# Optimization experiments

Measured on AMD Instinct MI355X. Metric: run time of the kernel, lower is better.

## Reference

```python
import jax, jax.numpy as jnp
import numpy as np

VOCAB, EMB, HID, NCLS, B, T = 50000, 32, 64, 3, 512, 512

def setup_inputs() -> dict:
    key = jax.random.key(0)
    ks = jax.random.split(key, 7)
    tokens = jax.random.randint(ks[0], (B, T), 0, VOCAB, dtype=jnp.int32)
    emb = jax.random.normal(ks[1], (VOCAB, EMB), dtype=jnp.float32) * 0.05
    # Keras LSTM weights: kernel [EMB, 4*HID], recurrent_kernel [HID, 4*HID], bias [4*HID]; gate order i,f,c,o
    Wk = jax.random.normal(ks[2], (EMB, 4 * HID), dtype=jnp.float32) * (1.0 / np.sqrt(EMB))
    Wr = jax.random.normal(ks[3], (HID, 4 * HID), dtype=jnp.float32) * (1.0 / np.sqrt(HID))
    b = jnp.zeros((4 * HID,), dtype=jnp.float32)
    Wd = jax.random.normal(ks[4], (HID, NCLS), dtype=jnp.float32) * (1.0 / np.sqrt(HID))
    bd = jnp.zeros((NCLS,), dtype=jnp.float32)
    return {"tokens": tokens, "emb": emb, "Wk": Wk, "Wr": Wr, "b": b, "Wd": Wd, "bd": bd}

def _lstm_last_hidden(x, Wk, Wr, b):
    # x: [B, T, EMB] -> last hidden state [B, HID]. Keras gate order: i, f, c(g), o.
    Bsz = x.shape[0]
    # Precompute input projections for all timesteps (one big GEMM): [T, B, 4H]
    xz = jnp.einsum('bte,eh->tbh', x, Wk) + b

    def step(carry, xzt):
        h, c = carry
        z = xzt + h @ Wr  # [B, 4H]
        i, f, g, o = jnp.split(z, 4, axis=-1)
        i = jax.nn.sigmoid(i)
        f = jax.nn.sigmoid(f)
        o = jax.nn.sigmoid(o)
        c = f * c + i * jnp.tanh(g)
        h = o * jnp.tanh(c)
        return (h, c), None

    h0 = jnp.zeros((Bsz, HID), dtype=x.dtype)
    c0 = jnp.zeros((Bsz, HID), dtype=x.dtype)
    (hT, _), _ = jax.lax.scan(step, (h0, c0), xz)
    return hT

def reference(tokens, emb, Wk, Wr, b, Wd, bd):
    x = emb[tokens]                      # [B, T, EMB] embedding lookup
    h = _lstm_last_hidden(x, Wk, Wr, b)  # [B, HID]
    # Dropout layers are identity at inference; Dense + softmax
    logits = h @ Wd + bd                 # [B, NCLS]
    return jax.nn.softmax(logits, axis=-1)
```

## Files before the change

kernel.cpp:

```cpp
#include <hip/hip_runtime.h>


#define VOCAB 50000
#define EMB 32
#define HID 64
#define NCLS 3
#define BATCH 512
#define TSEQ 512
#define FOURH 256
#define LOG2E 1.4426950408889634f
#define GSEQ 4
#define NBLK (BATCH / GSEQ)

typedef _Float16 half8 __attribute__((ext_vector_type(8)));
typedef float f32x4 __attribute__((ext_vector_type(4)));

#define MFMA16 __builtin_amdgcn_mfma_f32_16x16x32_f16
#define PKRTZ(a, b) __builtin_bit_cast(int, __builtin_amdgcn_cvt_pkrtz((a), (b)))

#define WAVE_BARRIER()                                        \
    {                                                         \
        asm volatile("s_waitcnt lgkmcnt(0)" ::: "memory");    \
        __builtin_amdgcn_s_barrier();                         \
    }

#define LSTM_STEP(CUR, TT, XW, XL)                                            \
    {                                                                         \
        const half8* ap = (const half8*)(hxc + (CUR) * 768 + abase);          \
        const half8 a0 = ap[0];                                               \
        const half8 a1 = ap[4];                                               \
        const half8 a2 = ap[8];                                               \
        if (li8) {                                                            \
            int2 st;                                                          \
            st.x = PKRTZ(XW.x, XW.y);                                         \
            st.y = PKRTZ(XW.z, XW.w);                                         \
            *(int2*)(hxc + ((CUR) ^ 1) * 768 + xwoff) = st;                   \
            const int tn2 = ((TT) + 2 < TSEQ) ? (TT) + 2 : TSEQ - 1;          \
            const int tk = toks[(w << 9) + tn2];                              \
            XL = *(const float4*)(emb + tk * EMB + (l << 2));                 \
        }                                                                     \
        f32x4 A0, A1, A2, A3, B0, B1, B2, B3, C0, C1, C2, C3;                 \
        A0 = MFMA16(a0, bfr[0][0], zz, 0, 0, 0);                              \
        A1 = MFMA16(a0, bfr[1][0], zz, 0, 0, 0);                              \
        A2 = MFMA16(a0, bfr[2][0], zz, 0, 0, 0);                              \
        A3 = MFMA16(a0, bfr[3][0], zz, 0, 0, 0);                              \
        B0 = MFMA16(a1, bfr[0][1], zz, 0, 0, 0);                              \
        B1 = MFMA16(a1, bfr[1][1], zz, 0, 0, 0);                              \
        B2 = MFMA16(a1, bfr[2][1], zz, 0, 0, 0);                              \
        B3 = MFMA16(a1, bfr[3][1], zz, 0, 0, 0);                              \
        C0 = MFMA16(a2, bfr[0][2], zz, 0, 0, 0);                              \
        C1 = MFMA16(a2, bfr[1][2], zz, 0, 0, 0);                              \
        C2 = MFMA16(a2, bfr[2][2], zz, 0, 0, 0);                              \
        C3 = MFMA16(a2, bfr[3][2], zz, 0, 0, 0);                              \
        const float zi = (A0[0] + B0[0]) + C0[0];                             \
        const float zf = (A1[0] + B1[0]) + C1[0];                             \
        const float zg = (A2[0] + B2[0]) + C2[0];                             \
        const float zo = (A3[0] + B3[0]) + C3[0];                             \
        const float si = __builtin_amdgcn_rcpf(                               \
            1.0f + __builtin_amdgcn_exp2f(fmaf(zi, -LOG2E, bci)));            \
        const float sf = __builtin_amdgcn_rcpf(                               \
            1.0f + __builtin_amdgcn_exp2f(fmaf(zf, -LOG2E, bcf)));            \
        const float sg = __builtin_amdgcn_rcpf(                               \
            1.0f + __builtin_amdgcn_exp2f(fmaf(zg, -2.0f * LOG2E, bcg)));     \
        const float so = __builtin_amdgcn_rcpf(                               \
            1.0f + __builtin_amdgcn_exp2f(fmaf(zo, -LOG2E, bco)));            \
        const float gt = fmaf(2.0f, sg, -1.0f);                               \
        cst = fmaf(sf, cst, si * gt);                                         \
        const float st2 = __builtin_amdgcn_rcpf(                              \
            1.0f + __builtin_amdgcn_exp2f(cst * (-2.0f * LOG2E)));            \
        const float th = fmaf(2.0f, st2, -1.0f);                              \
        const float hv = so * th;                                             \
        *(_Float16*)(hxc + ((CUR) ^ 1) * 768 + hwoff) = (_Float16)hv;         \
        WAVE_BARRIER()                                                        \
    }

__global__ __launch_bounds__(256)
void lstm_kernel(const int* __restrict__ tokens, const float* __restrict__ emb,
                 const float* __restrict__ Wk, const float* __restrict__ Wr,
                 const float* __restrict__ bias, const float* __restrict__ Wd,
                 const float* __restrict__ bd, float* __restrict__ out)
{
    __shared__ __align__(16) _Float16 hx[2][GSEQ][96];
    __shared__ int toks[GSEQ * TSEQ];

    const int tid = threadIdx.x;
    const int w   = tid >> 6;
    const int l   = tid & 63;
    const int li  = l & 15;
    const int q   = l >> 4;
    const bool li8 = (l < 8);
    const int s0  = blockIdx.x << 2;

    char* hxc = (char*)&hx[0][0][0];

    {
        const int4* src = (const int4*)(tokens + (s0 << 9));
        int4* dst = (int4*)toks;
        dst[tid] = src[tid];
        dst[tid + 256] = src[tid + 256];
    }

    if (tid < 64) {
        int2 z2; z2.x = 0; z2.y = 0;
        *(int2*)(hxc + (tid >> 4) * 192 + ((tid & 15) << 3)) = z2;
    }

    half8 bfr[4][3];
#pragma unroll
    for (int g = 0; g < 4; ++g) {
        const int col = (g << 6) + (w << 4) + li;
#pragma unroll
        for (int c2 = 0; c2 < 3; ++c2) {
#pragma unroll
            for (int i = 0; i < 8; ++i) {
                const int k = (c2 << 5) + (q << 3) + i;
                const float wv = (k < HID) ? Wr[k * FOURH + col]
                                           : Wk[(k - HID) * FOURH + col];
                bfr[g][c2][i] = (_Float16)wv;
            }
        }
    }

    const int u = (w << 4) + li;
    const float bci = -bias[u] * LOG2E;
    const float bcf = -bias[u + 64] * LOG2E;
    const float bcg = -bias[u + 128] * (2.0f * LOG2E);
    const float bco = -bias[u + 192] * LOG2E;

    const int abase = ((li >> 2) * 192) + (q << 4);
    const int hwoff = q * 192 + (u << 1);
    const int xwoff = w * 192 + 128 + (l << 3);

    __syncthreads();

    float4 xA = make_float4(0.f, 0.f, 0.f, 0.f);
    float4 xB = make_float4(0.f, 0.f, 0.f, 0.f);
    if (li8) {
        const int tk0 = toks[w << 9];
        const float4 x0 = *(const float4*)(emb + tk0 * EMB + (l << 2));
        int2 st;
        st.x = PKRTZ(x0.x, x0.y);
        st.y = PKRTZ(x0.z, x0.w);
        *(int2*)(hxc + xwoff) = st;
        const int tk1 = toks[(w << 9) + 1];
        xA = *(const float4*)(emb + tk1 * EMB + (l << 2));
    }
    __syncthreads();

    float cst = 0.0f;
    const f32x4 zz = {0.0f, 0.0f, 0.0f, 0.0f};

    for (int t = 0; t < TSEQ; t += 2) {
        LSTM_STEP(0, t, xA, xB)
        LSTM_STEP(1, t + 1, xB, xA)
    }

    if (tid < GSEQ) {
        const _Float16* hf = &hx[0][tid][0];
        float a0 = bd[0], a1 = bd[1], a2 = bd[2];
#pragma unroll 8
        for (int k = 0; k < HID; ++k) {
            const float hk = (float)hf[k];
            a0 = fmaf(hk, Wd[k * NCLS + 0], a0);
            a1 = fmaf(hk, Wd[k * NCLS + 1], a1);
            a2 = fmaf(hk, Wd[k * NCLS + 2], a2);
        }
        const float mm = fmaxf(a0, fmaxf(a1, a2));
        const float e0 = __expf(a0 - mm);
        const float e1 = __expf(a1 - mm);
        const float e2 = __expf(a2 - mm);
        const float den = e0 + e1 + e2;
        float* op = out + (s0 + tid) * NCLS;
        op[0] = e0 / den;
        op[1] = e1 / den;
        op[2] = e2 / den;
    }
}

extern "C" void kernel_launch(void* const* d_in, const int* in_sizes, int n_in,
                              void* d_out, int out_size, void* d_ws, size_t ws_size,
                              hipStream_t stream) {
    const int*   tokens = (const int*)  d_in[0];
    const float* emb    = (const float*)d_in[1];
    const float* Wk     = (const float*)d_in[2];
    const float* Wr     = (const float*)d_in[3];
    const float* b      = (const float*)d_in[4];
    const float* Wd     = (const float*)d_in[5];
    const float* bd     = (const float*)d_in[6];
    float* out = (float*)d_out;
    (void)d_ws; (void)ws_size; (void)in_sizes; (void)n_in; (void)out_size;

    lstm_kernel<<<dim3(NBLK), dim3(256), 0, stream>>>(
        tokens, emb, Wk, Wr, b, Wd, bd, out);
}
```

Before: 240.7 us.

## Process two interleaved sequence groups per block to expose ILP in recurrence

Each block now handles 8 sequences as two independent groups of 4. Every wave interleaves the MFMA and activation chains of both groups, which halves the grid to 64 blocks. The MFMAs now accumulate through the C operand instead of summing three separate results. The aim is to hide MFMA and transcendental latency in the serial timestep loop by overlapping two independent recurrences, at the cost of doubled per-step work per wave and a longer dependent MFMA chain.

```diff
diff --git a/kernel.cpp b/kernel.cpp
--- a/kernel.cpp
+++ b/kernel.cpp
@@ -9,8 +9,9 @@
 #define TSEQ 512
 #define FOURH 256
 #define LOG2E 1.4426950408889634f
-#define GSEQ 4
+#define GSEQ 8
 #define NBLK (BATCH / GSEQ)
+#define GSTRIDE 1536
 
 typedef _Float16 half8 __attribute__((ext_vector_type(8)));
 typedef float f32x4 __attribute__((ext_vector_type(4)));
@@ -24,38 +25,8 @@
         __builtin_amdgcn_s_barrier();                         \
     }
 
-#define LSTM_STEP(CUR, TT, XW, XL)                                            \
+#define ACT(zi, zf, zg, zo, cst, hv)                                          \
     {                                                                         \
-        const half8* ap = (const half8*)(hxc + (CUR) * 768 + abase);          \
-        const half8 a0 = ap[0];                                               \
-        const half8 a1 = ap[4];                                               \
-        const half8 a2 = ap[8];                                               \
-        if (li8) {                                                            \
-            int2 st;                                                          \
-            st.x = PKRTZ(XW.x, XW.y);                                         \
-            st.y = PKRTZ(XW.z, XW.w);                                         \
-            *(int2*)(hxc + ((CUR) ^ 1) * 768 + xwoff) = st;                   \
-            const int tn2 = ((TT) + 2 < TSEQ) ? (TT) + 2 : TSEQ - 1;          \
-            const int tk = toks[(w << 9) + tn2];                              \
-            XL = *(const float4*)(emb + tk * EMB + (l << 2));                 \
-        }                                                                     \
-        f32x4 A0, A1, A2, A3, B0, B1, B2, B3, C0, C1, C2, C3;                 \
-        A0 = MFMA16(a0, bfr[0][0], zz, 0, 0, 0);                              \
-        A1 = MFMA16(a0, bfr[1][0], zz, 0, 0, 0);                              \
-        A2 = MFMA16(a0, bfr[2][0], zz, 0, 0, 0);                              \
-        A3 = MFMA16(a0, bfr[3][0], zz, 0, 0, 0);                              \
-        B0 = MFMA16(a1, bfr[0][1], zz, 0, 0, 0);                              \
-        B1 = MFMA16(a1, bfr[1][1], zz, 0, 0, 0);                              \
-        B2 = MFMA16(a1, bfr[2][1], zz, 0, 0, 0);                              \
-        B3 = MFMA16(a1, bfr[3][1], zz, 0, 0, 0);                              \
-        C0 = MFMA16(a2, bfr[0][2], zz, 0, 0, 0);                              \
-        C1 = MFMA16(a2, bfr[1][2], zz, 0, 0, 0);                              \
-        C2 = MFMA16(a2, bfr[2][2], zz, 0, 0, 0);                              \
-        C3 = MFMA16(a2, bfr[3][2], zz, 0, 0, 0);                              \
-        const float zi = (A0[0] + B0[0]) + C0[0];                             \
-        const float zf = (A1[0] + B1[0]) + C1[0];                             \
-        const float zg = (A2[0] + B2[0]) + C2[0];                             \
-        const float zo = (A3[0] + B3[0]) + C3[0];                             \
         const float si = __builtin_amdgcn_rcpf(                               \
             1.0f + __builtin_amdgcn_exp2f(fmaf(zi, -LOG2E, bci)));            \
         const float sf = __builtin_amdgcn_rcpf(                               \
@@ -68,9 +39,65 @@
         cst = fmaf(sf, cst, si * gt);                                         \
         const float st2 = __builtin_amdgcn_rcpf(                              \
             1.0f + __builtin_amdgcn_exp2f(cst * (-2.0f * LOG2E)));            \
-        const float th = fmaf(2.0f, st2, -1.0f);                              \
-        const float hv = so * th;                                             \
-        *(_Float16*)(hxc + ((CUR) ^ 1) * 768 + hwoff) = (_Float16)hv;         \
+        hv = so * fmaf(2.0f, st2, -1.0f);                                     \
+    }
+
+#define LSTM_STEP(CUR, TT, XWA, XLA, XWB, XLB)                                \
+    {                                                                         \
+        const half8* apA = (const half8*)(hxc + (CUR) * 768 + abase);         \
+        const half8 a0A = apA[0];                                             \
+        const half8 a1A = apA[4];                                             \
+        const half8 a2A = apA[8];                                             \
+        const half8* apB = (const half8*)(hxc + GSTRIDE + (CUR) * 768 + abase);\
+        const half8 a0B = apB[0];                                             \
+        const half8 a1B = apB[4];                                             \
+        const half8 a2B = apB[8];                                             \
+        const int tn2 = ((TT) + 2 < TSEQ) ? (TT) + 2 : TSEQ - 1;              \
+        if (l < 8) {                                                          \
+            int2 st;                                                          \
+            st.x = PKRTZ(XWA.x, XWA.y);                                       \
+            st.y = PKRTZ(XWA.z, XWA.w);                                       \
+            *(int2*)(hxc + ((CUR) ^ 1) * 768 + xwoff) = st;                   \
+            const int tk = toks[(w << 9) + tn2];                              \
+            XLA = *(const float4*)(emb + tk * EMB + ((l & 7) << 2));          \
+        } else if (l < 16) {                                                  \
+            int2 st;                                                          \
+            st.x = PKRTZ(XWB.x, XWB.y);                                       \
+            st.y = PKRTZ(XWB.z, XWB.w);                                       \
+            *(int2*)(hxc + GSTRIDE + ((CUR) ^ 1) * 768 + xwoffB) = st;        \
+            const int tk = toks[((4 + w) << 9) + tn2];                        \
+            XLB = *(const float4*)(emb + tk * EMB + ((l & 7) << 2));          \
+        }                                                                     \
+        f32x4 zA0, zA1, zA2, zA3, zB0, zB1, zB2, zB3;                         \
+        zA0 = MFMA16(a0A, bfr[0][0], zz, 0, 0, 0);                            \
+        zA1 = MFMA16(a0A, bfr[1][0], zz, 0, 0, 0);                            \
+        zA2 = MFMA16(a0A, bfr[2][0], zz, 0, 0, 0);                            \
+        zA3 = MFMA16(a0A, bfr[3][0], zz, 0, 0, 0);                            \
+        zB0 = MFMA16(a0B, bfr[0][0], zz, 0, 0, 0);                            \
+        zB1 = MFMA16(a0B, bfr[1][0], zz, 0, 0, 0);                            \
+        zB2 = MFMA16(a0B, bfr[2][0], zz, 0, 0, 0);                            \
+        zB3 = MFMA16(a0B, bfr[3][0], zz, 0, 0, 0);                            \
+        zA0 = MFMA16(a1A, bfr[0][1], zA0, 0, 0, 0);                           \
+        zA1 = MFMA16(a1A, bfr[1][1], zA1, 0, 0, 0);                           \
+        zA2 = MFMA16(a1A, bfr[2][1], zA2, 0, 0, 0);                           \
+        zA3 = MFMA16(a1A, bfr[3][1], zA3, 0, 0, 0);                           \
+        zB0 = MFMA16(a1B, bfr[0][1], zB0, 0, 0, 0);                           \
+        zB1 = MFMA16(a1B, bfr[1][1], zB1, 0, 0, 0);                           \
+        zB2 = MFMA16(a1B, bfr[2][1], zB2, 0, 0, 0);                           \
+        zB3 = MFMA16(a1B, bfr[3][1], zB3, 0, 0, 0);                           \
+        zA0 = MFMA16(a2A, bfr[0][2], zA0, 0, 0, 0);                           \
+        zA1 = MFMA16(a2A, bfr[1][2], zA1, 0, 0, 0);                           \
+        zA2 = MFMA16(a2A, bfr[2][2], zA2, 0, 0, 0);                           \
+        zA3 = MFMA16(a2A, bfr[3][2], zA3, 0, 0, 0);                           \
+        zB0 = MFMA16(a2B, bfr[0][2], zB0, 0, 0, 0);                           \
+        zB1 = MFMA16(a2B, bfr[1][2], zB1, 0, 0, 0);                           \
+        zB2 = MFMA16(a2B, bfr[2][2], zB2, 0, 0, 0);                           \
+        zB3 = MFMA16(a2B, bfr[3][2], zB3, 0, 0, 0);                           \
+        float hvA, hvB;                                                       \
+        ACT(zA0[0], zA1[0], zA2[0], zA3[0], cstA, hvA)                        \
+        ACT(zB0[0], zB1[0], zB2[0], zB3[0], cstB, hvB)                        \
+        *(_Float16*)(hxc + ((CUR) ^ 1) * 768 + hwoff) = (_Float16)hvA;        \
+        *(_Float16*)(hxc + GSTRIDE + ((CUR) ^ 1) * 768 + hwoff) = (_Float16)hvB;\
         WAVE_BARRIER()                                                        \
     }
 
@@ -80,7 +107,7 @@
                  const float* __restrict__ bias, const float* __restrict__ Wd,
                  const float* __restrict__ bd, float* __restrict__ out)
 {
-    __shared__ __align__(16) _Float16 hx[2][GSEQ][96];
+    __shared__ __align__(16) _Float16 hx[2][2][4][96];
     __shared__ int toks[GSEQ * TSEQ];
 
     const int tid = threadIdx.x;
@@ -88,21 +115,23 @@
     const int l   = tid & 63;
     const int li  = l & 15;
     const int q   = l >> 4;
-    const bool li8 = (l < 8);
-    const int s0  = blockIdx.x << 2;
-
-    char* hxc = (char*)&hx[0][0][0];
+    const int s0  = blockIdx.x << 3;
+
+    char* hxc = (char*)&hx[0][0][0][0];
 
     {
-        const int4* src = (const int4*)(tokens + (s0 << 9));
+        const int4* src = (const int4*)(tokens + ((long)s0 << 9));
         int4* dst = (int4*)toks;
-        dst[tid] = src[tid];
+        dst[tid]       = src[tid];
         dst[tid + 256] = src[tid + 256];
-    }
-
-    if (tid < 64) {
+        dst[tid + 512] = src[tid + 512];
+        dst[tid + 768] = src[tid + 768];
+    }
+
+    if (tid < 128) {
         int2 z2; z2.x = 0; z2.y = 0;
-        *(int2*)(hxc + (tid >> 4) * 192 + ((tid & 15) << 3)) = z2;
+        *(int2*)(hxc + (tid >> 6) * GSTRIDE + (((tid >> 4) & 3) * 192) +
+                 ((tid & 15) << 3)) = z2;
     }
 
     half8 bfr[4][3];
@@ -127,36 +156,49 @@
     const float bcg = -bias[u + 128] * (2.0f * LOG2E);
     const float bco = -bias[u + 192] * LOG2E;
 
-    const int abase = ((li >> 2) * 192) + (q << 4);
-    const int hwoff = q * 192 + (u << 1);
-    const int xwoff = w * 192 + 128 + (l << 3);
+    const int abase  = ((li >> 2) * 192) + (q << 4);
+    const int hwoff  = q * 192 + (u << 1);
+    const int xwoff  = w * 192 + 128 + ((l & 7) << 3);
+    const int xwoffB = w * 192 + 128 + ((l & 7) << 3);
 
     __syncthreads();
 
-    float4 xA = make_float4(0.f, 0.f, 0.f, 0.f);
-    float4 xB = make_float4(0.f, 0.f, 0.f, 0.f);
-    if (li8) {
+    float4 xA1 = make_float4(0.f, 0.f, 0.f, 0.f);
+    float4 xA2 = make_float4(0.f, 0.f, 0.f, 0.f);
+    float4 xB1 = make_float4(0.f, 0.f, 0.f, 0.f);
+    float4 xB2 = make_float4(0.f, 0.f, 0.f, 0.f);
+    if (l < 8) {
         const int tk0 = toks[w << 9];
-        const float4 x0 = *(const float4*)(emb + tk0 * EMB + (l << 2));
+        const float4 x0 = *(const float4*)(emb + tk0 * EMB + ((l & 7) << 2));
         int2 st;
         st.x = PKRTZ(x0.x, x0.y);
         st.y = PKRTZ(x0.z, x0.w);
         *(int2*)(hxc + xwoff) = st;
         const int tk1 = toks[(w << 9) + 1];
-        xA = *(const float4*)(emb + tk1 * EMB + (l << 2));
+        xA1 = *(const float4*)(emb + tk1 * EMB + ((l & 7) << 2));
+    } else if (l < 16) {
+        const int tk0 = toks[(4 + w) << 9];
+        const float4 x0 = *(const float4*)(emb + tk0 * EMB + ((l & 7) << 2));
+        int2 st;
+        st.x = PKRTZ(x0.x, x0.y);
+        st.y = PKRTZ(x0.z, x0.w);
+        *(int2*)(hxc + GSTRIDE + xwoffB) = st;
+        const int tk1 = toks[((4 + w) << 9) + 1];
+        xB1 = *(const float4*)(emb + tk1 * EMB + ((l & 7) << 2));
     }
     __syncthreads();
 
-    float cst = 0.0f;
+    float cstA = 0.0f, cstB = 0.0f;
     const f32x4 zz = {0.0f, 0.0f, 0.0f, 0.0f};
 
     for (int t = 0; t < TSEQ; t += 2) {
-        LSTM_STEP(0, t, xA, xB)
-        LSTM_STEP(1, t + 1, xB, xA)
+        LSTM_STEP(0, t,     xA1, xA2, xB1, xB2)
+        LSTM_STEP(1, t + 1, xA2, xA1, xB2, xB1)
     }
 
     if (tid < GSEQ) {
-        const _Float16* hf = &hx[0][tid][0];
+        const _Float16* hf =
+            (const _Float16*)(hxc + (tid >> 2) * GSTRIDE + (tid & 3) * 192);
         float a0 = bd[0], a1 = bd[1], a2 = bd[2];
 #pragma unroll 8
         for (int k = 0; k < HID; ++k) {
```

Measured after the change: 447.2 us. 1.86x slower.

## Restructure LSTM kernel to 16 sequences per block with accumulated MFMA chain

Applied to the files above, without the earlier changes.

Each block now handles 16 sequences with 1024 threads (16 waves, 4 hidden units each), and the gate layout is changed so one accumulated chain of three MFMAs yields all four gates for a lane, replacing twelve independent MFMAs plus adds. Embedding rows are fetched directly from global memory by every lane with a token prefetch distance of four, dropping the shared-memory token copy. When workspace is available, a pre-kernel converts the embedding table to fp16 so the recurrent loop loads half-width rows. This trades a serial MFMA dependency chain and a larger block-wide barrier per step for higher MFMA utilisation and fewer blocks, plus an extra conversion kernel over the whole table.

```diff
diff --git a/kernel.cpp b/kernel.cpp
--- a/kernel.cpp
+++ b/kernel.cpp
@@ -9,8 +9,10 @@
 #define TSEQ 512
 #define FOURH 256
 #define LOG2E 1.4426950408889634f
-#define GSEQ 4
+#define GSEQ 16
 #define NBLK (BATCH / GSEQ)
+#define ROWB 144
+#define BUFB (GSEQ * ROWB)
 
 typedef _Float16 half8 __attribute__((ext_vector_type(8)));
 typedef float f32x4 __attribute__((ext_vector_type(4)));
@@ -24,139 +26,141 @@
         __builtin_amdgcn_s_barrier();                         \
     }
 
-#define LSTM_STEP(CUR, TT, XW, XL)                                            \
+__global__ __launch_bounds__(256)
+void build_emb16(const float* __restrict__ emb, _Float16* __restrict__ emb16) {
+    const int idx = blockIdx.x * 256 + threadIdx.x;
+    if (idx >= (VOCAB * EMB) / 8) return;
+    const float4* src = (const float4*)(emb + (long)idx * 8);
+    const float4 a = src[0], b = src[1];
+    int4 o;
+    o.x = PKRTZ(a.x, a.y);
+    o.y = PKRTZ(a.z, a.w);
+    o.z = PKRTZ(b.x, b.y);
+    o.w = PKRTZ(b.z, b.w);
+    ((int4*)emb16)[idx] = o;
+}
+
+#define LSTM_STEP(CUR, TT, XR, TKR)                                           \
     {                                                                         \
-        const half8* ap = (const half8*)(hxc + (CUR) * 768 + abase);          \
-        const half8 a0 = ap[0];                                               \
-        const half8 a1 = ap[4];                                               \
-        const half8 a2 = ap[8];                                               \
-        if (li8) {                                                            \
-            int2 st;                                                          \
-            st.x = PKRTZ(XW.x, XW.y);                                         \
-            st.y = PKRTZ(XW.z, XW.w);                                         \
-            *(int2*)(hxc + ((CUR) ^ 1) * 768 + xwoff) = st;                   \
-            const int tn2 = ((TT) + 2 < TSEQ) ? (TT) + 2 : TSEQ - 1;          \
-            const int tk = toks[(w << 9) + tn2];                              \
-            XL = *(const float4*)(emb + tk * EMB + (l << 2));                 \
+        const half8 b0 = *(const half8*)(hxc + (CUR) * BUFB + bbase);         \
+        const half8 b1 = *(const half8*)(hxc + (CUR) * BUFB + bbase + 64);    \
+        const half8 xcur = XR;                                                \
+        if (TAB) {                                                            \
+            XR = *(const half8*)(emb16 + (long)TKR * EMB + (q << 3));         \
+        } else {                                                              \
+            const float4* xp = (const float4*)(emb + (long)TKR * EMB + (q << 3)); \
+            const float4 xa = xp[0], xb = xp[1];                              \
+            int4 pk;                                                          \
+            pk.x = PKRTZ(xa.x, xa.y);                                         \
+            pk.y = PKRTZ(xa.z, xa.w);                                         \
+            pk.z = PKRTZ(xb.x, xb.y);                                         \
+            pk.w = PKRTZ(xb.z, xb.w);                                         \
+            XR = __builtin_bit_cast(half8, pk);                               \
         }                                                                     \
-        f32x4 A0, A1, A2, A3, B0, B1, B2, B3, C0, C1, C2, C3;                 \
-        A0 = MFMA16(a0, bfr[0][0], zz, 0, 0, 0);                              \
-        A1 = MFMA16(a0, bfr[1][0], zz, 0, 0, 0);                              \
-        A2 = MFMA16(a0, bfr[2][0], zz, 0, 0, 0);                              \
-        A3 = MFMA16(a0, bfr[3][0], zz, 0, 0, 0);                              \
-        B0 = MFMA16(a1, bfr[0][1], zz, 0, 0, 0);                              \
-        B1 = MFMA16(a1, bfr[1][1], zz, 0, 0, 0);                              \
-        B2 = MFMA16(a1, bfr[2][1], zz, 0, 0, 0);                              \
-        B3 = MFMA16(a1, bfr[3][1], zz, 0, 0, 0);                              \
-        C0 = MFMA16(a2, bfr[0][2], zz, 0, 0, 0);                              \
-        C1 = MFMA16(a2, bfr[1][2], zz, 0, 0, 0);                              \
-        C2 = MFMA16(a2, bfr[2][2], zz, 0, 0, 0);                              \
-        C3 = MFMA16(a2, bfr[3][2], zz, 0, 0, 0);                              \
-        const float zi = (A0[0] + B0[0]) + C0[0];                             \
-        const float zf = (A1[0] + B1[0]) + C1[0];                             \
-        const float zg = (A2[0] + B2[0]) + C2[0];                             \
-        const float zo = (A3[0] + B3[0]) + C3[0];                             \
+        const int tn4 = ((TT) + 4 < TSEQ) ? (TT) + 4 : TSEQ - 1;              \
+        TKR = tokp[tn4];                                                      \
+        f32x4 acc;                                                            \
+        acc = MFMA16(wf0, b0, zz, 0, 0, 0);                                   \
+        acc = MFMA16(wf1, b1, acc, 0, 0, 0);                                  \
+        acc = MFMA16(wf2, xcur, acc, 0, 0, 0);                                \
         const float si = __builtin_amdgcn_rcpf(                               \
-            1.0f + __builtin_amdgcn_exp2f(fmaf(zi, -LOG2E, bci)));            \
+            1.0f + __builtin_amdgcn_exp2f(fmaf(acc[0], -LOG2E, bci)));        \
         const float sf = __builtin_amdgcn_rcpf(                               \
-            1.0f + __builtin_amdgcn_exp2f(fmaf(zf, -LOG2E, bcf)));            \
+            1.0f + __builtin_amdgcn_exp2f(fmaf(acc[1], -LOG2E, bcf)));        \
         const float sg = __builtin_amdgcn_rcpf(                               \
-            1.0f + __builtin_amdgcn_exp2f(fmaf(zg, -2.0f * LOG2E, bcg)));     \
+            1.0f + __builtin_amdgcn_exp2f(fmaf(acc[2], -2.0f * LOG2E, bcg))); \
         const float so = __builtin_amdgcn_rcpf(                               \
-            1.0f + __builtin_amdgcn_exp2f(fmaf(zo, -LOG2E, bco)));            \
+            1.0f + __builtin_amdgcn_exp2f(fmaf(acc[3], -LOG2E, bco)));        \
         const float gt = fmaf(2.0f, sg, -1.0f);                               \
         cst = fmaf(sf, cst, si * gt);                                         \
         const float st2 = __builtin_amdgcn_rcpf(                              \
             1.0f + __builtin_amdgcn_exp2f(cst * (-2.0f * LOG2E)));            \
-        const float th = fmaf(2.0f, st2, -1.0f);                              \
-        const float hv = so * th;                                             \
-        *(_Float16*)(hxc + ((CUR) ^ 1) * 768 + hwoff) = (_Float16)hv;         \
+        const float hv = so * fmaf(2.0f, st2, -1.0f);                         \
+        *(_Float16*)(hxc + ((CUR) ^ 1) * BUFB + hwoff) = (_Float16)hv;        \
         WAVE_BARRIER()                                                        \
     }
 
-__global__ __launch_bounds__(256)
+template <bool TAB>
+__global__ __launch_bounds__(1024)
 void lstm_kernel(const int* __restrict__ tokens, const float* __restrict__ emb,
                  const float* __restrict__ Wk, const float* __restrict__ Wr,
                  const float* __restrict__ bias, const float* __restrict__ Wd,
-                 const float* __restrict__ bd, float* __restrict__ out)
+                 const float* __restrict__ bd, const _Float16* __restrict__ emb16,
+                 float* __restrict__ out)
 {
-    __shared__ __align__(16) _Float16 hx[2][GSEQ][96];
-    __shared__ int toks[GSEQ * TSEQ];
+    __shared__ __align__(16) _Float16 hx[2][GSEQ][ROWB / 2];
 
     const int tid = threadIdx.x;
     const int w   = tid >> 6;
     const int l   = tid & 63;
-    const int li  = l & 15;
+    const int s   = l & 15;
     const int q   = l >> 4;
-    const bool li8 = (l < 8);
-    const int s0  = blockIdx.x << 2;
+    const int s0  = blockIdx.x << 4;
 
     char* hxc = (char*)&hx[0][0][0];
 
+    if (tid < 128) {
+        int4 z4; z4.x = 0; z4.y = 0; z4.z = 0; z4.w = 0;
+        *(int4*)(hxc + (tid >> 3) * ROWB + ((tid & 7) << 4)) = z4;
+    }
+
+    half8 wf0, wf1, wf2;
     {
-        const int4* src = (const int4*)(tokens + (s0 << 9));
-        int4* dst = (int4*)toks;
-        dst[tid] = src[tid];
-        dst[tid + 256] = src[tid + 256];
-    }
-
-    if (tid < 64) {
-        int2 z2; z2.x = 0; z2.y = 0;
-        *(int2*)(hxc + (tid >> 4) * 192 + ((tid & 15) << 3)) = z2;
-    }
-
-    half8 bfr[4][3];
+        const int g   = s & 3;
+        const int col = (g << 6) + (w << 2) + (s >> 2);
 #pragma unroll
-    for (int g = 0; g < 4; ++g) {
-        const int col = (g << 6) + (w << 4) + li;
-#pragma unroll
-        for (int c2 = 0; c2 < 3; ++c2) {
-#pragma unroll
-            for (int i = 0; i < 8; ++i) {
-                const int k = (c2 << 5) + (q << 3) + i;
-                const float wv = (k < HID) ? Wr[k * FOURH + col]
-                                           : Wk[(k - HID) * FOURH + col];
-                bfr[g][c2][i] = (_Float16)wv;
-            }
+        for (int i = 0; i < 8; ++i) {
+            const int kq = (q << 3) + i;
+            wf0[i] = (_Float16)Wr[kq * FOURH + col];
+            wf1[i] = (_Float16)Wr[(32 + kq) * FOURH + col];
+            wf2[i] = (_Float16)Wk[kq * FOURH + col];
         }
     }
 
-    const int u = (w << 4) + li;
+    const int u = (w << 2) + q;
     const float bci = -bias[u] * LOG2E;
     const float bcf = -bias[u + 64] * LOG2E;
     const float bcg = -bias[u + 128] * (2.0f * LOG2E);
     const float bco = -bias[u + 192] * LOG2E;
 
-    const int abase = ((li >> 2) * 192) + (q << 4);
-    const int hwoff = q * 192 + (u << 1);
-    const int xwoff = w * 192 + 128 + (l << 3);
-
-    __syncthreads();
-
-    float4 xA = make_float4(0.f, 0.f, 0.f, 0.f);
-    float4 xB = make_float4(0.f, 0.f, 0.f, 0.f);
-    if (li8) {
-        const int tk0 = toks[w << 9];
-        const float4 x0 = *(const float4*)(emb + tk0 * EMB + (l << 2));
-        int2 st;
-        st.x = PKRTZ(x0.x, x0.y);
-        st.y = PKRTZ(x0.z, x0.w);
-        *(int2*)(hxc + xwoff) = st;
-        const int tk1 = toks[(w << 9) + 1];
-        xA = *(const float4*)(emb + tk1 * EMB + (l << 2));
-    }
+    const int bbase = s * ROWB + (q << 4);
+    const int hwoff = s * ROWB + (u << 1);
+
+    const int* tokp = tokens + (long)(s0 + s) * TSEQ;
+    int tkA = tokp[0];
+    int tkB = tokp[1];
+    half8 x0, x1;
+    if (TAB) {
+        x0 = *(const half8*)(emb16 + (long)tkA * EMB + (q << 3));
+        x1 = *(const half8*)(emb16 + (long)tkB * EMB + (q << 3));
+    } else {
+        const float4* p0 = (const float4*)(emb + (long)tkA * EMB + (q << 3));
+        const float4 a0 = p0[0], a1 = p0[1];
+        int4 pk;
+        pk.x = PKRTZ(a0.x, a0.y); pk.y = PKRTZ(a0.z, a0.w);
+        pk.z = PKRTZ(a1.x, a1.y); pk.w = PKRTZ(a1.z, a1.w);
+        x0 = __builtin_bit_cast(half8, pk);
+        const float4* p1 = (const float4*)(emb + (long)tkB * EMB + (q << 3));
+        const float4 b0 = p1[0], b1 = p1[1];
+        pk.x = PKRTZ(b0.x, b0.y); pk.y = PKRTZ(b0.z, b0.w);
+        pk.z = PKRTZ(b1.x, b1.y); pk.w = PKRTZ(b1.z, b1.w);
+        x1 = __builtin_bit_cast(half8, pk);
+    }
+    tkA = tokp[2];
+    tkB = tokp[3];
+
     __syncthreads();
 
     float cst = 0.0f;
     const f32x4 zz = {0.0f, 0.0f, 0.0f, 0.0f};
 
     for (int t = 0; t < TSEQ; t += 2) {
-        LSTM_STEP(0, t, xA, xB)
-        LSTM_STEP(1, t + 1, xB, xA)
+        LSTM_STEP(0, t,     x0, tkA)
+        LSTM_STEP(1, t + 1, x1, tkB)
     }
 
     if (tid < GSEQ) {
-        const _Float16* hf = &hx[0][tid][0];
+        const _Float16* hf = (const _Float16*)(hxc + tid * ROWB);
         float a0 = bd[0], a1 = bd[1], a2 = bd[2];
 #pragma unroll 8
         for (int k = 0; k < HID; ++k) {
@@ -188,8 +192,17 @@
     const float* Wd     = (const float*)d_in[5];
     const float* bd     = (const float*)d_in[6];
     float* out = (float*)d_out;
-    (void)d_ws; (void)ws_size; (void)in_sizes; (void)n_in; (void)out_size;
-
-    lstm_kernel<<<dim3(NBLK), dim3(256), 0, stream>>>(
-        tokens, emb, Wk, Wr, b, Wd, bd, out);
+    (void)in_sizes; (void)n_in; (void)out_size;
+
+    const size_t need = (size_t)VOCAB * EMB * sizeof(_Float16);
+    if (ws_size >= need) {
+        _Float16* emb16 = (_Float16*)d_ws;
+        build_emb16<<<dim3((VOCAB * EMB / 8 + 255) / 256), dim3(256), 0, stream>>>(
+            emb, emb16);
+        lstm_kernel<true><<<dim3(NBLK), dim3(1024), 0, stream>>>(
+            tokens, emb, Wk, Wr, b, Wd, bd, emb16, out);
+    } else {
+        lstm_kernel<false><<<dim3(NBLK), dim3(1024), 0, stream>>>(
+            tokens, emb, Wk, Wr, b, Wd, bd, nullptr, out);
+    }
 }
```

Result: slower. 450.5 us (+87.2%).
